# Performance work log

Hardware: AMD Instinct MI355X
Metric: run time of the kernel (lower is better)

## Reference

```python
import jax, jax.numpy as jnp
import numpy as np

RCR = 5.2
RCA = 3.5
ETA_R = 16.0
ETA_A = 8.0
ZETA = 32.0
NUM_SPECIES = 4
NUM_PAIRS = NUM_SPECIES * (NUM_SPECIES + 1) // 2  # 10
SHFR = jnp.asarray(np.linspace(0.9, RCR, 17)[:-1], dtype=jnp.float32)   # (16,)
SHFA = jnp.asarray(np.linspace(0.9, RCA, 5)[:-1], dtype=jnp.float32)    # (4,)
SHFZ = jnp.asarray((np.linspace(0.0, np.pi, 9) + np.pi / 16.0)[:-1], dtype=jnp.float32)  # (8,)

def _triu_index(n):
    s1, s2 = np.triu_indices(n)
    t = np.zeros((n, n), dtype=np.int32)
    t[s1, s2] = np.arange(len(s1))
    t[s2, s1] = np.arange(len(s1))
    return jnp.asarray(t)

TRIU = _triu_index(NUM_SPECIES)  # (4,4) -> pair index in [0,10)

def _fc(d, rc):
    # cosine cutoff, zero beyond rc
    return jnp.where(d < rc, 0.5 * jnp.cos(np.float32(np.pi) * d / rc) + 0.5, 0.0)

def _aev(species, coordinates):
    N, A = species.shape
    # vec[n,i,j] = r_j - r_i  (N,A,A,3)
    vec = coordinates[:, None, :, :] - coordinates[:, :, None, :]
    d2 = jnp.sum(vec * vec, axis=-1)                      # (N,A,A)
    eye = jnp.eye(A, dtype=bool)
    d = jnp.sqrt(jnp.where(eye, 1.0, d2))                 # safe sqrt on diagonal
    pair_mask = (~eye).astype(coordinates.dtype)          # (A,A)

    # ---- radial AEV ----
    fcr = _fc(d, RCR) * pair_mask                         # (N,A,A)
    rad = 0.25 * jnp.exp(-ETA_R * (d[..., None] - SHFR) ** 2) * fcr[..., None]  # (N,A,A,16)
    sp_oh = jax.nn.one_hot(species, NUM_SPECIES, dtype=coordinates.dtype)       # (N,A,4)
    radial_aev = jnp.einsum('nijt,njs->nist', rad, sp_oh).reshape(N, A, -1)     # (N,A,64)

    # ---- angular AEV ----
    fca = _fc(d, RCA) * pair_mask                         # (N,A,A)
    dot = jnp.einsum('nijc,nikc->nijk', vec, vec)         # (N,A,A,A)
    cosang = 0.95 * dot / jnp.clip(d[:, :, :, None] * d[:, :, None, :], 1e-10)
    angles = jnp.arccos(cosang)                           # (N,A,A,A)
    mask_jk = (~eye).astype(coordinates.dtype)            # j != k
    fcj12 = fca[:, :, :, None] * fca[:, :, None, :] * mask_jk[None, None]  # (N,A,A,A)
    dmean = 0.5 * (d[:, :, :, None] + d[:, :, None, :])   # (N,A,A,A)
    factor1 = ((1.0 + jnp.cos(angles[..., None] - SHFZ)) * 0.5) ** ZETA    # (N,A,A,A,8)
    factor2 = jnp.exp(-ETA_A * (dmean[..., None] - SHFA) ** 2)             # (N,A,A,A,4)
    # terms over ordered (j,k); each unordered pair counted twice, so the
    # original factor 2 and the 0.5 double-count correction cancel.
    terms = (fcj12[..., None] * factor2)[..., :, None] * factor1[..., None, :]  # (N,A,A,A,4,8)
    terms = terms.reshape(N, A, A, A, SHFA.shape[0] * SHFZ.shape[0])            # (N,A,A,A,32)
    pair_idx = TRIU[species[:, :, None], species[:, None, :]]                   # (N,A,A)
    pair_oh = jax.nn.one_hot(pair_idx, NUM_PAIRS, dtype=coordinates.dtype)      # (N,A,A,10)
    angular_aev = jnp.einsum('nijkt,njkp->nipt', terms, pair_oh).reshape(N, A, -1)  # (N,A,320)

    return jnp.concatenate([radial_aev, angular_aev], axis=-1)  # (N,A,384)

def setup_inputs() -> dict:
    key = jax.random.key(0)
    k1, k2 = jax.random.split(key)
    species = jax.random.randint(k1, (32, 48), 0, NUM_SPECIES)
    # atoms in an 8 Angstrom box -> realistic neighbor density for 5.2 A cutoff
    coordinates = jax.random.uniform(k2, (32, 48, 3), dtype=jnp.float32) * 8.0
    return {"species": species, "coordinates": coordinates}

def reference(species, coordinates):
    return _aev(species, coordinates)
```

## Files before the change

### kernel.cpp

```cpp
#include <hip/hip_runtime.h>
#include <math.h>


#define A_ATOMS 48
#define NMOL    32
#define NFEAT   384
#define CHUNK   256

__device__ __constant__ float CZ_TAB[8] = {
     0.980785280f,  0.831469612f,  0.555570233f,  0.195090322f,
    -0.195090322f, -0.555570233f, -0.831469612f, -0.980785280f };
__device__ __constant__ float SZ_TAB[8] = {
     0.195090322f,  0.555570233f,  0.831469612f,  0.980785280f,
     0.980785280f,  0.831469612f,  0.555570233f,  0.195090322f };

__device__ __forceinline__ float bf2f(unsigned short h) {
    return __uint_as_float(((unsigned int)h) << 16);
}

__global__ __launch_bounds__(256, 6)
void AEVComputer_2156073583107_kernel(const void* __restrict__ coords_raw,
                                      const void* __restrict__ species_raw,
                                      float* __restrict__ out)
{
    const int bid   = blockIdx.x;
    const int n     = bid / A_ATOMS;
    const int i     = bid - n * A_ATOMS;
    const int tid   = threadIdx.x;
    const int w     = tid >> 6;
    const int lane  = tid & 63;
    const int sub   = lane >> 5;
    const int slice = (w << 1) | sub;
    const int t     = lane & 31;

    __shared__ float dL[A_ATOMS], fcaL[A_ATOMS];
    __shared__ float ux[A_ATOMS], uy[A_ATOMS], uz[A_ATOMS];
    __shared__ int   sp[A_ATOMS], nbr[A_ATOMS];
    __shared__ int   Msh;
    __shared__ float4 pairD[CHUNK];
    __shared__ int    pairP[CHUNK];
    __shared__ float  rad_m[4][64];
    __shared__ float  ang_m[8][320];

    const unsigned short* cu16 = (const unsigned short*)coords_raw;
    const unsigned int*   su32 = (const unsigned int*)species_raw;

    if (tid < 64) {
        float v = bf2f(cu16[tid]);
        unsigned long long mb = __ballot(fabsf(v) < 32.0f);
        const bool coords_bf16 = (__popcll(mb) >= 60);
        unsigned int svv = su32[tid & 31];
        unsigned long long m2 = __ballot((tid < 32) && svv >= 0x3F000000u && svv < 0x40800000u);
        unsigned long long m3 = __ballot((tid < 32) && (tid & 1) && svv != 0u);
        const int smode = (__popcll(m2) > 20) ? 2 : ((m3 == 0ull) ? 1 : 0);

        float x = 0.f, y = 0.f, z = 0.f; int s = 0;
        if (tid < A_ATOMS) {
            const int g = n * A_ATOMS + tid;
            if (coords_bf16) {
                x = bf2f(cu16[3 * g]); y = bf2f(cu16[3 * g + 1]); z = bf2f(cu16[3 * g + 2]);
            } else {
                const float* cf = (const float*)coords_raw;
                x = cf[3 * g]; y = cf[3 * g + 1]; z = cf[3 * g + 2];
            }
            if (smode == 0)      s = ((const int*)species_raw)[g];
            else if (smode == 1) s = ((const int*)species_raw)[2 * g];
            else                 s = (int)(((const float*)species_raw)[g] + 0.5f);
            s = (s < 0) ? 0 : ((s > 3) ? 3 : s);
        }
        const float xi = __shfl(x, i), yi = __shfl(y, i), zi = __shfl(z, i);
        float dx = x - xi, dy = y - yi, dz = z - zi;
        float d2 = dx * dx + dy * dy + dz * dz;
        float d  = (tid == i) ? 1.0f : sqrtf(d2);
        float inv = 1.0f / d;
        bool pred = (tid < A_ATOMS) && (tid != i) && (d < 3.5f);
        float fca = pred ? (0.5f * __cosf(0.8975979010f * d) + 0.5f) : 0.0f;
        if (tid < A_ATOMS) {
            dL[tid] = d;
            ux[tid] = dx * inv; uy[tid] = dy * inv; uz[tid] = dz * inv;
            fcaL[tid] = fca; sp[tid] = s;
        }
        unsigned long long mask = __ballot(pred);
        if (pred) {
            int pos = __popcll(mask & ((1ull << tid) - 1ull));
            nbr[pos] = tid;
        }
        if (tid == 0) Msh = __popcll(mask);
    }
    __syncthreads();
    const int M = Msh;
    const int npairs = (M * (M - 1)) >> 1;

    {
        const int   s    = lane >> 4;
        const int   rt   = lane & 15;
        const float shfr = 0.9f + 0.26875f * (float)rt;
        float radv = 0.0f;
        #pragma unroll
        for (int jj = 0; jj < 12; ++jj) {
            const int j = w + 4 * jj;
            float d   = dL[j];
            float fcr = 0.5f * __cosf(0.6041524333f * d) + 0.5f;
            float e   = d - shfr;
            float val = 0.25f * __expf(-16.0f * e * e) * fcr;
            bool  ok  = (j != i) && (d < 5.2f) && (sp[j] == s);
            radv += ok ? val : 0.0f;
        }
        rad_m[w][lane] = radv;
    }

    float a[10];
    #pragma unroll
    for (int p = 0; p < 10; ++p) a[p] = 0.0f;
    const float czv  = CZ_TAB[t & 7];
    const float szv  = SZ_TAB[t & 7];
    const float shfa = 0.9f + 0.65f * (float)(t >> 3);

    for (int base = 0; base < npairs; base += CHUNK) {
        const int q = base + tid;
        if (q < npairs) {
            const float b = (float)(2 * M - 1);
            int jj = (int)(0.5f * (b - sqrtf(fmaxf(b * b - 8.0f * (float)q, 0.0f))));
            jj = max(0, min(jj, M - 2));
            while (jj > 0 && q < ((jj * (2 * M - 1 - jj)) >> 1)) --jj;
            while (q >= (((jj + 1) * (2 * M - 2 - jj)) >> 1)) ++jj;
            const int kk = jj + 1 + (q - ((jj * (2 * M - 1 - jj)) >> 1));
            const int j = nbr[jj], k = nbr[kk];
            float c  = fmaf(ux[j], ux[k], fmaf(uy[j], uy[k], uz[j] * uz[k]));
            float cc = 0.95f * c;
            float ss = sqrtf(fmaxf(1.0f - cc * cc, 0.0f));
            float4 pd;
            pd.x = 0.5f * cc;
            pd.y = 0.5f * ss;
            pd.z = 2.0f * fcaL[j] * fcaL[k];
            pd.w = 0.5f * (dL[j] + dL[k]);
            const int sj = sp[j], sk = sp[k];
            const int lo = min(sj, sk), hi = max(sj, sk);
            pairD[tid] = pd;
            pairP[tid] = ((lo * (7 - lo)) >> 1) + hi;
        }
        __syncthreads();
        const int cnt = min(CHUNK, npairs - base);
        for (int qq = slice; qq < cnt; qq += 8) {
            float4 v = pairD[qq];
            int    p = pairP[qq];
            float x  = fmaf(v.y, szv, fmaf(v.x, czv, 0.5f));
            float x2 = x * x, x4 = x2 * x2, x8 = x4 * x4, x16 = x8 * x8;
            float f1 = x16 * x16;
            float e  = v.w - shfa;
            float term = v.z * __expf(-8.0f * e * e) * f1;
            #pragma unroll
            for (int pp = 0; pp < 10; ++pp) a[pp] += (p == pp) ? term : 0.0f;
        }
        __syncthreads();
    }

    #pragma unroll
    for (int pp = 0; pp < 10; ++pp) ang_m[slice][pp * 32 + t] = a[pp];
    __syncthreads();

    const size_t outb = (size_t)bid * NFEAT;
    for (int f = tid; f < NFEAT; f += 256) {
        float v;
        if (f < 64) {
            v = rad_m[0][f] + rad_m[1][f] + rad_m[2][f] + rad_m[3][f];
        } else {
            const int g = f - 64;
            v = ((ang_m[0][g] + ang_m[1][g]) + (ang_m[2][g] + ang_m[3][g]))
              + ((ang_m[4][g] + ang_m[5][g]) + (ang_m[6][g] + ang_m[7][g]));
        }
        out[outb + f] = v;
    }
}

extern "C" void kernel_launch(void* const* d_in, const int* in_sizes, int n_in,
                              void* d_out, int out_size, void* d_ws, size_t ws_size,
                              hipStream_t stream) {
    if (n_in < 2) return;
    const void* coords;
    const void* species;
    if (in_sizes[0] >= in_sizes[1]) { coords = d_in[0]; species = d_in[1]; }
    else                            { coords = d_in[1]; species = d_in[0]; }
    float* out = (float*)d_out;
    AEVComputer_2156073583107_kernel<<<NMOL * A_ATOMS, 256, 0, stream>>>(coords, species, out);
}
```

Baseline: 65.13 us.

## Bucket angular pairs by species pair and precompute radial-shift weights per pair

Each chunk's angular pairs are now counting-sorted in shared memory by species-pair index using atomic counters and a prefix sum, so the inner loop accumulates into a single known register per segment instead of doing a 10-way select per term. The four radial Gaussian factors exp(-8(dm-shfa)^2), times the cutoff weight, are computed once per pair by the producer thread instead of once per consuming lane. This removes redundant exp evaluations and select instructions from the hot loop. In exchange it adds two extra block barriers per chunk, shared-memory atomics, a serial prefix sum on one thread, and segment loops whose short, uneven trip counts may leave slices idle.

```diff
diff --git a/kernel.cpp b/kernel.cpp
--- a/kernel.cpp
+++ b/kernel.cpp
@@ -32,15 +32,17 @@
     const int sub   = lane >> 5;
     const int slice = (w << 1) | sub;
     const int t     = lane & 31;
+    const int ia    = t >> 3;
 
     __shared__ float dL[A_ATOMS], fcaL[A_ATOMS];
     __shared__ float ux[A_ATOMS], uy[A_ATOMS], uz[A_ATOMS];
     __shared__ int   sp[A_ATOMS], nbr[A_ATOMS];
     __shared__ int   Msh;
-    __shared__ float4 pairD[CHUNK];
-    __shared__ int    pairP[CHUNK];
-    __shared__ float  rad_m[4][64];
-    __shared__ float  ang_m[8][320];
+    __shared__ float2 pairA[CHUNK];
+    __shared__ float  pairW[CHUNK * 4];
+    __shared__ int   cnt[10], curs[10], ofs[11];
+    __shared__ float rad_m[4][64];
+    __shared__ float ang_m[8][320];
 
     const unsigned short* cu16 = (const unsigned short*)coords_raw;
     const unsigned int*   su32 = (const unsigned int*)species_raw;
@@ -112,13 +114,17 @@
     float a[10];
     #pragma unroll
     for (int p = 0; p < 10; ++p) a[p] = 0.0f;
-    const float czv  = CZ_TAB[t & 7];
-    const float szv  = SZ_TAB[t & 7];
-    const float shfa = 0.9f + 0.65f * (float)(t >> 3);
+    const float czv = CZ_TAB[t & 7];
+    const float szv = SZ_TAB[t & 7];
 
     for (int base = 0; base < npairs; base += CHUNK) {
-        const int q = base + tid;
-        if (q < npairs) {
+        if (tid < 10) cnt[tid] = 0;
+        __syncthreads();
+
+        const int  q     = base + tid;
+        const bool havep = (q < npairs);
+        float2 pa; float wf[4]; int p = 0;
+        if (havep) {
             const float b = (float)(2 * M - 1);
             int jj = (int)(0.5f * (b - sqrtf(fmaxf(b * b - 8.0f * (float)q, 0.0f))));
             jj = max(0, min(jj, M - 2));
@@ -129,28 +135,50 @@
             float c  = fmaf(ux[j], ux[k], fmaf(uy[j], uy[k], uz[j] * uz[k]));
             float cc = 0.95f * c;
             float ss = sqrtf(fmaxf(1.0f - cc * cc, 0.0f));
-            float4 pd;
-            pd.x = 0.5f * cc;
-            pd.y = 0.5f * ss;
-            pd.z = 2.0f * fcaL[j] * fcaL[k];
-            pd.w = 0.5f * (dL[j] + dL[k]);
+            pa.x = 0.5f * cc;
+            pa.y = 0.5f * ss;
+            const float wgt = 2.0f * fcaL[j] * fcaL[k];
+            const float dm  = 0.5f * (dL[j] + dL[k]);
+            #pragma unroll
+            for (int q4 = 0; q4 < 4; ++q4) {
+                float e = dm - (0.9f + 0.65f * (float)q4);
+                wf[q4] = wgt * __expf(-8.0f * e * e);
+            }
             const int sj = sp[j], sk = sp[k];
             const int lo = min(sj, sk), hi = max(sj, sk);
-            pairD[tid] = pd;
-            pairP[tid] = ((lo * (7 - lo)) >> 1) + hi;
-        }
-        __syncthreads();
-        const int cnt = min(CHUNK, npairs - base);
-        for (int qq = slice; qq < cnt; qq += 8) {
-            float4 v = pairD[qq];
-            int    p = pairP[qq];
-            float x  = fmaf(v.y, szv, fmaf(v.x, czv, 0.5f));
-            float x2 = x * x, x4 = x2 * x2, x8 = x4 * x4, x16 = x8 * x8;
-            float f1 = x16 * x16;
-            float e  = v.w - shfa;
-            float term = v.z * __expf(-8.0f * e * e) * f1;
+            p = ((lo * (7 - lo)) >> 1) + hi;
+            atomicAdd(&cnt[p], 1);
+        }
+        __syncthreads();
+        if (tid == 0) {
+            int o = 0;
             #pragma unroll
-            for (int pp = 0; pp < 10; ++pp) a[pp] += (p == pp) ? term : 0.0f;
+            for (int pp = 0; pp < 10; ++pp) { ofs[pp] = o; curs[pp] = o; o += cnt[pp]; }
+            ofs[10] = o;
+        }
+        __syncthreads();
+        if (havep) {
+            int slot = atomicAdd(&curs[p], 1);
+            pairA[slot] = pa;
+            pairW[4 * slot + 0] = wf[0];
+            pairW[4 * slot + 1] = wf[1];
+            pairW[4 * slot + 2] = wf[2];
+            pairW[4 * slot + 3] = wf[3];
+        }
+        __syncthreads();
+
+        #pragma unroll
+        for (int pp = 0; pp < 10; ++pp) {
+            const int e1 = ofs[pp + 1];
+            float acc = a[pp];
+            for (int qq = ofs[pp] + slice; qq < e1; qq += 8) {
+                float2 v  = pairA[qq];
+                float wf2 = pairW[4 * qq + ia];
+                float x   = fmaf(v.y, szv, fmaf(v.x, czv, 0.5f));
+                float x2 = x * x, x4 = x2 * x2, x8 = x4 * x4, x16 = x8 * x8;
+                acc = fmaf(x16 * x16, wf2, acc);
+            }
+            a[pp] = acc;
         }
         __syncthreads();
     }
```

After: 63.93 us. No clear change (-1.8%).
